# Performance work log

Measured on AMD Instinct MI355X. Metric: run time of the kernel, lower is better.

The kernel has to match this reference:

```python
import jax, jax.numpy as jnp
import numpy as np

N = 50000
F_IN = 512
H1, C1 = 8, 16          # layer-1 heads / per-head channels
H2, C2 = 1, 40          # layer-2 heads / num_classes
NEG_SLOPE = 0.2


def setup_inputs() -> dict:
    key = jax.random.key(0)
    ks = jax.random.split(key, 10)
    E = 800000
    x = jax.random.normal(ks[0], (N, F_IN), dtype=jnp.float32)
    edge_index = jax.random.randint(ks[1], (2, E), 0, N, dtype=jnp.int64)
    s1 = 1.0 / np.sqrt(F_IN)
    s2 = 1.0 / np.sqrt(H1 * C1)
    return {
        "x": x,
        "edge_index": edge_index,
        "W1": jax.random.normal(ks[2], (F_IN, H1 * C1), dtype=jnp.float32) * s1,
        "att_src1": jax.random.normal(ks[3], (H1, C1), dtype=jnp.float32) * s2,
        "att_dst1": jax.random.normal(ks[4], (H1, C1), dtype=jnp.float32) * s2,
        "b1": jnp.zeros((H1 * C1,), dtype=jnp.float32),
        "W2": jax.random.normal(ks[5], (H1 * C1, H2 * C2), dtype=jnp.float32) * s2,
        "att_src2": jax.random.normal(ks[6], (H2, C2), dtype=jnp.float32) * (1.0 / np.sqrt(C2)),
        "att_dst2": jax.random.normal(ks[7], (H2, C2), dtype=jnp.float32) * (1.0 / np.sqrt(C2)),
        "b2": jnp.zeros((H2 * C2,), dtype=jnp.float32),
    }


def _gat_conv(x, W, att_src, att_dst, b, src, dst, H, C):
    # x: [N, Fin] -> h: [N, H, C]
    h = (x @ W).reshape(N, H, C)
    a_src = jnp.einsum("nhc,hc->nh", h, att_src)  # [N, H]
    a_dst = jnp.einsum("nhc,hc->nh", h, att_dst)
    e = a_src[src] + a_dst[dst]                    # [E, H]
    e = jax.nn.leaky_relu(e, NEG_SLOPE)
    # segment softmax over edges sharing the same target node (dst)
    m = jax.ops.segment_max(e, dst, num_segments=N)         # [N, H]
    ex = jnp.exp(e - m[dst])
    denom = jax.ops.segment_sum(ex, dst, num_segments=N)    # [N, H]
    alpha = ex / (denom[dst] + 1e-16)                        # [E, H]
    msg = h[src] * alpha[..., None]                          # [E, H, C]
    out = jax.ops.segment_sum(msg, dst, num_segments=N)     # [N, H, C]
    return out.reshape(N, H * C) + b


def reference(x, edge_index, W1, att_src1, att_dst1, b1, W2, att_src2, att_dst2, b2):
    # add self-loops (PyG GATConv default)
    loop = jnp.arange(N, dtype=edge_index.dtype)
    src = jnp.concatenate([edge_index[0], loop])
    dst = jnp.concatenate([edge_index[1], loop])
    h = _gat_conv(x, W1, att_src1, att_dst1, b1, src, dst, H1, C1)
    h = jax.nn.elu(h)
    h = _gat_conv(h, W2, att_src2, att_dst2, b2, src, dst, H2, C2)
    return jax.nn.log_softmax(h, axis=1)
```

## Files before the change

### kernel.cpp

```cpp
#include <hip/hip_runtime.h>
#include <math.h>

#define N_NODES 50000
#define FIN 512
#define NE 800000
#define ETOT 850000
#define F1 128
#define H1 8
#define F2 40
#define BCAP 64
#define NBIN 196
#define BINCAP 6144

typedef __attribute__((ext_vector_type(8))) short bf16x8;
typedef __attribute__((ext_vector_type(4))) float f32x4;

__device__ inline ushort f2bf(float f){
  union{float f; unsigned u;} v; v.f=f;
  return (ushort)((v.u + 0x8000u) >> 16);
}
__device__ inline float bflo(uint u){ union{uint a;float f;} v; v.a = u << 16;         return v.f; }
__device__ inline float bfhi(uint u){ union{uint a;float f;} v; v.a = u & 0xffff0000u; return v.f; }
__device__ inline float bf1(ushort u){ union{uint a;float f;} v; v.a = ((uint)u) << 16; return v.f; }

__device__ inline bf16x8 cvt8(float4 a, float4 b){
  union{ushort u[8]; bf16x8 v;} r;
  r.u[0]=f2bf(a.x); r.u[1]=f2bf(a.y); r.u[2]=f2bf(a.z); r.u[3]=f2bf(a.w);
  r.u[4]=f2bf(b.x); r.u[5]=f2bf(b.y); r.u[6]=f2bf(b.z); r.u[7]=f2bf(b.w);
  return r.v;
}


__global__ __launch_bounds__(1024) void k_binA(const int* __restrict__ src, const int* __restrict__ dst,
                                               int* __restrict__ binCursor, uint* __restrict__ binbuf){
  __shared__ int hist[256];
  __shared__ int base[256];
  int t = threadIdx.x;
  if(t < 256) hist[t] = 0;
  __syncthreads();

  uint pk[8]; int bn[8];
  int i0 = blockIdx.x*8192 + t;
  #pragma unroll
  for(int k=0;k<8;k++){
    int i = i0 + k*1024;
    int d = -1, s = 0;
    if(i < NE){ d = dst[i]; s = src[i]; }
    else if(i < ETOT){ d = i - NE; s = d; }
    if(d >= 0){
      bn[k] = d >> 8;
      pk[k] = ((uint)d << 16) | (uint)s;
      atomicAdd(&hist[bn[k]], 1);
    } else bn[k] = -1;
  }
  __syncthreads();
  if(t < 256){
    int h = hist[t];
    base[t] = (t < NBIN && h > 0) ? atomicAdd(&binCursor[t], h) : 0;
  }
  __syncthreads();
  if(t < 256) hist[t] = 0;
  __syncthreads();
  #pragma unroll
  for(int k=0;k<8;k++){
    if(bn[k] >= 0){
      int off = atomicAdd(&hist[bn[k]], 1);
      binbuf[(size_t)bn[k]*BINCAP + base[bn[k]] + off] = pk[k];
    }
  }
}


__global__ __launch_bounds__(1024) void k_binB(const int* __restrict__ binCursor, const uint* __restrict__ binbuf,
                                               int* __restrict__ cnt, ushort* __restrict__ bucket){
  __shared__ int lcnt[256];
  __shared__ ushort lb[256][BCAP];
  int b = blockIdx.x, t = threadIdx.x;
  if(t < 256) lcnt[t] = 0;
  __syncthreads();
  int m = min(binCursor[b], BINCAP);
  const uint* p = binbuf + (size_t)b*BINCAP;
  for(int i=t; i<m; i+=1024){
    uint pk = p[i];
    int dl = (pk >> 16) & 255;
    int pos = atomicAdd(&lcnt[dl], 1);
    if(pos < BCAP) lb[dl][pos] = (ushort)(pk & 0xFFFF);
  }
  __syncthreads();
  int n0 = b << 8;
  int nrows = min(256, N_NODES - n0);
  if(t < nrows) cnt[n0 + t] = lcnt[t];
  const uint4* s4 = (const uint4*)lb;
  uint4* d4 = (uint4*)(bucket + (size_t)n0*BCAP);
  int total = nrows * 8;
  for(int i=t; i<total; i+=1024) d4[i] = s4[i];
}


__global__ __launch_bounds__(256) void k_cvtW12(const float* __restrict__ W1, const float* __restrict__ W2,
                                                ushort* __restrict__ Wtb, ushort* __restrict__ Wt2){
  int id = blockIdx.x*256 + threadIdx.x;
  if(id < 65536){
    int k = id >> 7, n = id & 127;
    Wtb[(size_t)(k>>3)*1024 + n*8 + (k&7)] = f2bf(W1[id]);
  } else {
    int id2 = id - 65536;
    if(id2 >= 6144) return;
    int j = id2 & 7;
    int t = id2 >> 3;
    int n = t % 48;
    int t2 = t / 48;
    int quad = t2 & 3, ks = t2 >> 2;
    int k = ks*32 + quad*8 + j;
    Wt2[id2] = (n < F2) ? f2bf(W2[k*F2 + n]) : (ushort)0;
  }
}


__global__ __launch_bounds__(256) void k_gemm1(const float* __restrict__ x, const ushort* __restrict__ Wtb,
                                               const float* __restrict__ as_w, const float* __restrict__ ad_w,
                                               ushort* __restrict__ h1b,
                                               float* __restrict__ a_src, float* __restrict__ a_dst){
  __shared__ ushort Asm[2][32][72];
  int tid  = threadIdx.x;
  int wave = tid >> 6, lane = tid & 63;
  int l15 = lane & 15, quad = lane >> 4;
  int bx = blockIdx.x;

  f32x4 acc[2][2];
  #pragma unroll
  for(int i=0;i<2;i++)
    #pragma unroll
    for(int j=0;j<2;j++) acc[i][j] = (f32x4){0.f,0.f,0.f,0.f};

  int am  = tid >> 3;
  int ak8 = (tid & 7) << 3;
  int agr = bx*32 + am;
  int agrc = min(agr, N_NODES-1);
  const float* xrow = x + (size_t)agrc*FIN + ak8;

  {
    float4 a0 = *(const float4*)xrow;
    float4 a1 = *(const float4*)(xrow + 4);
    *(bf16x8*)&Asm[0][am][ak8] = cvt8(a0, a1);
  }

  const ushort* wpB = Wtb + (size_t)quad*1024 + (size_t)(wave*32 + l15)*8;

  bf16x8 bcur[2][2];
  #pragma unroll
  for(int ks=0;ks<2;ks++)
    #pragma unroll
    for(int tn=0;tn<2;tn++)
      bcur[ks][tn] = *(const bf16x8*)(wpB + ks*4096 + tn*128);
  __syncthreads();

  for(int kt=0; kt<FIN; kt+=64){
    int cur = (kt >> 6) & 1;
    bool hn = (kt + 64) < FIN;

    float4 a0, a1;
    if(hn){
      a0 = *(const float4*)(xrow + kt + 64);
      a1 = *(const float4*)(xrow + kt + 68);
    }
    bf16x8 bnext[2][2];
    if(hn){
      #pragma unroll
      for(int ks=0;ks<2;ks++)
        #pragma unroll
        for(int tn=0;tn<2;tn++)
          bnext[ks][tn] = *(const bf16x8*)(wpB + (size_t)(kt+64)*128 + ks*4096 + tn*128);
    }

    bf16x8 af[2][2];
    #pragma unroll
    for(int tm=0;tm<2;tm++)
      #pragma unroll
      for(int ks=0;ks<2;ks++)
        af[tm][ks] = *(bf16x8*)&Asm[cur][tm*16 + l15][ks*32 + quad*8];

    #pragma unroll
    for(int ks=0;ks<2;ks++)
      #pragma unroll
      for(int tm=0;tm<2;tm++)
        #pragma unroll
        for(int tn=0;tn<2;tn++)
          acc[tm][tn] = __builtin_amdgcn_mfma_f32_16x16x32_bf16(af[tm][ks], bcur[ks][tn], acc[tm][tn], 0,0,0);

    if(hn)
      *(bf16x8*)&Asm[cur^1][am][ak8] = cvt8(a0, a1);
    __syncthreads();
    #pragma unroll
    for(int ks=0;ks<2;ks++)
      #pragma unroll
      for(int tn=0;tn<2;tn++)
        bcur[ks][tn] = bnext[ks][tn];
  }

  float wsv[2], wdv[2];
  #pragma unroll
  for(int tn=0;tn<2;tn++){
    int h = wave*2 + tn;
    wsv[tn] = as_w[h*16 + l15];
    wdv[tn] = ad_w[h*16 + l15];
  }

  #pragma unroll
  for(int tm=0;tm<2;tm++){
    #pragma unroll
    for(int r=0;r<4;r++){
      int row = bx*32 + tm*16 + quad*4 + r;
      bool ok = row < N_NODES;
      #pragma unroll
      for(int tn=0;tn<2;tn++){
        float v = acc[tm][tn][r];
        if(ok){
          int col = wave*32 + tn*16 + l15;
          h1b[(size_t)row*F1 + col] = f2bf(v);
        }
        float ss = v * wsv[tn];
        float dd = v * wdv[tn];
        #pragma unroll
        for(int m=8;m;m>>=1){ ss += __shfl_xor(ss, m); dd += __shfl_xor(dd, m); }
        if(ok && l15 == 0){
          int h = wave*2 + tn;
          a_src[(size_t)row*H1 + h] = ss;
          a_dst[(size_t)row*H1 + h] = dd;
        }
      }
    }
  }
}


__global__ __launch_bounds__(256) void k_agg1(const ushort* __restrict__ h1b, const float* __restrict__ a_src,
                                              const float* __restrict__ a_dst,
                                              const int* __restrict__ cnt, const ushort* __restrict__ bucket,
                                              const float* __restrict__ b1, ushort* __restrict__ gb){
  int wave = threadIdx.x >> 6, lane = threadIdx.x & 63;
  int n = blockIdx.x*4 + wave;
  if(n >= N_NODES) return;
  int hl = lane >> 3;
  float adv = a_dst[n*H1 + hl];
  int deg = min(cnt[n], BCAP);
  int sv = (int)bucket[(n << 6) + lane];
  const uint* h1u = (const uint*)h1b;

  float ws0=0.f, ax0=0.f, ay0=0.f;
  float ws1=0.f, ax1=0.f, ay1=0.f;
  float ws2=0.f, ax2=0.f, ay2=0.f;
  float ws3=0.f, ax3=0.f, ay3=0.f;
  int j = 0;
  for(; j+3<deg; j+=4){
    int s0 = __shfl(sv, j),   s1 = __shfl(sv, j+1);
    int s2 = __shfl(sv, j+2), s3 = __shfl(sv, j+3);
    float e0 = a_src[s0*H1 + hl] + adv;
    float e1 = a_src[s1*H1 + hl] + adv;
    float e2 = a_src[s2*H1 + hl] + adv;
    float e3 = a_src[s3*H1 + hl] + adv;
    e0 = e0 > 0.f ? e0 : 0.2f*e0;  e1 = e1 > 0.f ? e1 : 0.2f*e1;
    e2 = e2 > 0.f ? e2 : 0.2f*e2;  e3 = e3 > 0.f ? e3 : 0.2f*e3;
    float w0=__expf(e0), w1=__expf(e1), w2=__expf(e2), w3=__expf(e3);
    uint u0 = h1u[(size_t)s0*64 + lane];
    uint u1 = h1u[(size_t)s1*64 + lane];
    uint u2 = h1u[(size_t)s2*64 + lane];
    uint u3 = h1u[(size_t)s3*64 + lane];
    ax0 += w0*bflo(u0); ay0 += w0*bfhi(u0); ws0 += w0;
    ax1 += w1*bflo(u1); ay1 += w1*bfhi(u1); ws1 += w1;
    ax2 += w2*bflo(u2); ay2 += w2*bfhi(u2); ws2 += w2;
    ax3 += w3*bflo(u3); ay3 += w3*bfhi(u3); ws3 += w3;
  }
  for(; j<deg; j++){
    int s0 = __shfl(sv, j);
    float e0 = a_src[s0*H1 + hl] + adv;
    e0 = e0 > 0.f ? e0 : 0.2f*e0;
    float w0 = __expf(e0);
    uint u0 = h1u[(size_t)s0*64 + lane];
    ax0 += w0*bflo(u0); ay0 += w0*bfhi(u0); ws0 += w0;
  }
  float wsum = (ws0+ws1)+(ws2+ws3);
  float inv = 1.f/(wsum + 1e-16f);
  int c0 = lane*2;
  float o0 = ((ax0+ax1)+(ax2+ax3))*inv + b1[c0];
  float o1 = ((ay0+ay1)+(ay2+ay3))*inv + b1[c0+1];
  o0 = o0 > 0.f ? o0 : expm1f(o0);
  o1 = o1 > 0.f ? o1 : expm1f(o1);
  uint up = (uint)f2bf(o0) | ((uint)f2bf(o1) << 16);
  ((uint*)gb)[(size_t)n*64 + lane] = up;
}


__global__ __launch_bounds__(256) void k_gemm2(const ushort* __restrict__ gb, const ushort* __restrict__ Wt2,
                                               const float* __restrict__ as_w, const float* __restrict__ ad_w,
                                               ushort* __restrict__ h2b,
                                               float* __restrict__ a_src, float* __restrict__ a_dst){
  int tid = threadIdx.x;
  int wave = tid >> 6, lane = tid & 63;
  int l15 = lane & 15, quad = lane >> 4;
  int row0 = blockIdx.x*64 + wave*16;
  int arow = min(row0 + l15, N_NODES-1);
  const ushort* ap = gb + (size_t)arow*F1 + quad*8;

  f32x4 acc[3];
  #pragma unroll
  for(int tn=0;tn<3;tn++) acc[tn] = (f32x4){0.f,0.f,0.f,0.f};

  #pragma unroll
  for(int ks=0;ks<4;ks++){
    bf16x8 af = *(const bf16x8*)(ap + ks*32);
    #pragma unroll
    for(int tn=0;tn<3;tn++){
      bf16x8 bf = *(const bf16x8*)(Wt2 + ((size_t)(ks*4+quad)*48 + tn*16 + l15)*8);
      acc[tn] = __builtin_amdgcn_mfma_f32_16x16x32_bf16(af, bf, acc[tn], 0,0,0);
    }
  }

  float ws2v[3], wd2v[3];
  #pragma unroll
  for(int tn=0;tn<3;tn++){
    int col = tn*16 + l15;
    ws2v[tn] = (col < F2) ? as_w[col] : 0.f;
    wd2v[tn] = (col < F2) ? ad_w[col] : 0.f;
  }

  #pragma unroll
  for(int r=0;r<4;r++){
    int row = row0 + quad*4 + r;
    bool ok = row < N_NODES;
    float ss = 0.f, dd = 0.f;
    #pragma unroll
    for(int tn=0;tn<3;tn++){
      float v = acc[tn][r];
      int col = tn*16 + l15;
      if(ok && col < F2) h2b[(size_t)row*F2 + col] = f2bf(v);
      ss += v * ws2v[tn];
      dd += v * wd2v[tn];
    }
    #pragma unroll
    for(int m=8;m;m>>=1){ ss += __shfl_xor(ss, m); dd += __shfl_xor(dd, m); }
    if(ok && l15 == 0){
      a_src[row] = ss;
      a_dst[row] = dd;
    }
  }
}


__global__ __launch_bounds__(256) void k_agg2(const ushort* __restrict__ h2b, const float* __restrict__ a_src,
                                              const float* __restrict__ a_dst,
                                              const int* __restrict__ cnt, const ushort* __restrict__ bucket,
                                              const float* __restrict__ b2, float* __restrict__ out){
  int wave = threadIdx.x >> 6, lane = threadIdx.x & 63;
  int n = blockIdx.x*4 + wave;
  if(n >= N_NODES) return;
  float adv = a_dst[n];
  int deg = min(cnt[n], BCAP);
  int sv = (int)bucket[(n << 6) + lane];
  int c = (lane < F2) ? lane : (F2-1);

  float ws0=0.f, ac0=0.f, ws1=0.f, ac1=0.f, ws2=0.f, ac2=0.f, ws3=0.f, ac3=0.f;
  int j = 0;
  for(; j+3<deg; j+=4){
    int s0 = __shfl(sv, j),   s1 = __shfl(sv, j+1);
    int s2 = __shfl(sv, j+2), s3 = __shfl(sv, j+3);
    float e0 = a_src[s0] + adv, e1 = a_src[s1] + adv;
    float e2 = a_src[s2] + adv, e3 = a_src[s3] + adv;
    e0 = e0 > 0.f ? e0 : 0.2f*e0;  e1 = e1 > 0.f ? e1 : 0.2f*e1;
    e2 = e2 > 0.f ? e2 : 0.2f*e2;  e3 = e3 > 0.f ? e3 : 0.2f*e3;
    float w0=__expf(e0), w1=__expf(e1), w2=__expf(e2), w3=__expf(e3);
    ac0 += w0*bf1(h2b[(size_t)s0*F2 + c]); ws0 += w0;
    ac1 += w1*bf1(h2b[(size_t)s1*F2 + c]); ws1 += w1;
    ac2 += w2*bf1(h2b[(size_t)s2*F2 + c]); ws2 += w2;
    ac3 += w3*bf1(h2b[(size_t)s3*F2 + c]); ws3 += w3;
  }
  for(; j<deg; j++){
    int s0 = __shfl(sv, j);
    float e0 = a_src[s0] + adv;
    e0 = e0 > 0.f ? e0 : 0.2f*e0;
    float w0 = __expf(e0);
    ac0 += w0*bf1(h2b[(size_t)s0*F2 + c]); ws0 += w0;
  }
  float v = ((ac0+ac1)+(ac2+ac3))/(((ws0+ws1)+(ws2+ws3)) + 1e-16f) + b2[c];
  float mv = (lane < F2) ? v : -INFINITY;
  #pragma unroll
  for(int off=32; off; off>>=1) mv = fmaxf(mv, __shfl_xor(mv, off));
  float ex = (lane < F2) ? __expf(v - mv) : 0.f;
  #pragma unroll
  for(int off=32; off; off>>=1) ex += __shfl_xor(ex, off);
  if(lane < F2) out[(size_t)n*F2 + lane] = v - mv - logf(ex);
}


extern "C" void kernel_launch(void* const* d_in, const int* in_sizes, int n_in,
                              void* d_out, int out_size, void* d_ws, size_t ws_size,
                              hipStream_t stream) {
  const float* x        = (const float*)d_in[0];
  const int*   eidx     = (const int*)d_in[1];
  const float* W1       = (const float*)d_in[2];
  const float* att_src1 = (const float*)d_in[3];
  const float* att_dst1 = (const float*)d_in[4];
  const float* b1       = (const float*)d_in[5];
  const float* W2       = (const float*)d_in[6];
  const float* att_src2 = (const float*)d_in[7];
  const float* att_dst2 = (const float*)d_in[8];
  const float* b2       = (const float*)d_in[9];
  float* out = (float*)d_out;

  const int* src = eidx;
  const int* dst = eidx + NE;

  ushort* h1b  = (ushort*)d_ws;
  ushort* h2b  = h1b + 6400000;
  ushort* gb   = h2b + 2000000;
  ushort* Wtb  = gb + 6400000;
  ushort* bucket = Wtb + 65536;
  float* a_src1 = (float*)(bucket + 3200000);
  float* a_dst1 = a_src1 + 400000;
  float* a_src2 = a_dst1 + 400000;
  float* a_dst2 = a_src2 + 50000;
  int* cnt      = (int*)(a_dst2 + 50000);
  int* binCursor= cnt + 50002;
  uint* binbuf  = (uint*)(binCursor + 256);
  ushort* Wt2   = (ushort*)(binbuf + (size_t)NBIN*BINCAP);

  hipMemsetAsync(binCursor, 0, NBIN*sizeof(int), stream);
  k_binA<<<(ETOT+8191)/8192, 1024, 0, stream>>>(src, dst, binCursor, binbuf);
  k_binB<<<NBIN, 1024, 0, stream>>>(binCursor, binbuf, cnt, bucket);

  k_cvtW12<<<280, 256, 0, stream>>>(W1, W2, Wtb, Wt2);
  k_gemm1 <<<(N_NODES+31)/32, 256, 0, stream>>>(x, Wtb, att_src1, att_dst1, h1b, a_src1, a_dst1);
  k_agg1  <<<(N_NODES+3)/4, 256, 0, stream>>>(h1b, a_src1, a_dst1, cnt, bucket, b1, gb);

  k_gemm2 <<<(N_NODES+63)/64, 256, 0, stream>>>(gb, Wt2, att_src2, att_dst2, h2b, a_src2, a_dst2);
  k_agg2  <<<(N_NODES+3)/4, 256, 0, stream>>>(h2b, a_src2, a_dst2, cnt, bucket, b2, out);
}
```

Baseline: 289.3 us.

## Split each node's edge aggregation across four waves with LDS reduction

Both aggregation kernels now assign one block per destination node instead of one wave per node. The node's edge list is split evenly across the four waves, and their partial sums are combined through shared memory before wave 0 finishes the normalisation and writes the output. The aim is more memory-level parallelism per node and shorter serial gather chains. The cost is a block-wide barrier per node, a quarter as many nodes per block, and fewer edges per wave (about 17 per node on average) to amortise the per-node setup.

```diff
diff --git a/kernel.cpp b/kernel.cpp
--- a/kernel.cpp
+++ b/kernel.cpp
@@ -238,8 +238,9 @@
                                               const float* __restrict__ a_dst,
                                               const int* __restrict__ cnt, const ushort* __restrict__ bucket,
                                               const float* __restrict__ b1, ushort* __restrict__ gb){
+  __shared__ float pws[4][64], pax[4][64], pay[4][64];
   int wave = threadIdx.x >> 6, lane = threadIdx.x & 63;
-  int n = blockIdx.x*4 + wave;
+  int n = blockIdx.x;
   if(n >= N_NODES) return;
   int hl = lane >> 3;
   float adv = a_dst[n*H1 + hl];
@@ -247,12 +248,15 @@
   int sv = (int)bucket[(n << 6) + lane];
   const uint* h1u = (const uint*)h1b;
 
+  int q  = (deg + 3) >> 2;
+  int j0 = wave*q, j1 = min(j0 + q, deg);
+
   float ws0=0.f, ax0=0.f, ay0=0.f;
   float ws1=0.f, ax1=0.f, ay1=0.f;
   float ws2=0.f, ax2=0.f, ay2=0.f;
   float ws3=0.f, ax3=0.f, ay3=0.f;
-  int j = 0;
-  for(; j+3<deg; j+=4){
+  int j = j0;
+  for(; j+3<j1; j+=4){
     int s0 = __shfl(sv, j),   s1 = __shfl(sv, j+1);
     int s2 = __shfl(sv, j+2), s3 = __shfl(sv, j+3);
     float e0 = a_src[s0*H1 + hl] + adv;
@@ -271,7 +275,7 @@
     ax2 += w2*bflo(u2); ay2 += w2*bfhi(u2); ws2 += w2;
     ax3 += w3*bflo(u3); ay3 += w3*bfhi(u3); ws3 += w3;
   }
-  for(; j<deg; j++){
+  for(; j<j1; j++){
     int s0 = __shfl(sv, j);
     float e0 = a_src[s0*H1 + hl] + adv;
     e0 = e0 > 0.f ? e0 : 0.2f*e0;
@@ -279,15 +283,23 @@
     uint u0 = h1u[(size_t)s0*64 + lane];
     ax0 += w0*bflo(u0); ay0 += w0*bfhi(u0); ws0 += w0;
   }
-  float wsum = (ws0+ws1)+(ws2+ws3);
-  float inv = 1.f/(wsum + 1e-16f);
-  int c0 = lane*2;
-  float o0 = ((ax0+ax1)+(ax2+ax3))*inv + b1[c0];
-  float o1 = ((ay0+ay1)+(ay2+ay3))*inv + b1[c0+1];
-  o0 = o0 > 0.f ? o0 : expm1f(o0);
-  o1 = o1 > 0.f ? o1 : expm1f(o1);
-  uint up = (uint)f2bf(o0) | ((uint)f2bf(o1) << 16);
-  ((uint*)gb)[(size_t)n*64 + lane] = up;
+  pws[wave][lane] = (ws0+ws1)+(ws2+ws3);
+  pax[wave][lane] = (ax0+ax1)+(ax2+ax3);
+  pay[wave][lane] = (ay0+ay1)+(ay2+ay3);
+  __syncthreads();
+  if(wave == 0){
+    float W  = (pws[0][lane]+pws[1][lane]) + (pws[2][lane]+pws[3][lane]);
+    float AX = (pax[0][lane]+pax[1][lane]) + (pax[2][lane]+pax[3][lane]);
+    float AY = (pay[0][lane]+pay[1][lane]) + (pay[2][lane]+pay[3][lane]);
+    float inv = 1.f/(W + 1e-16f);
+    int c0 = lane*2;
+    float o0 = AX*inv + b1[c0];
+    float o1 = AY*inv + b1[c0+1];
+    o0 = o0 > 0.f ? o0 : expm1f(o0);
+    o1 = o1 > 0.f ? o1 : expm1f(o1);
+    uint up = (uint)f2bf(o0) | ((uint)f2bf(o1) << 16);
+    ((uint*)gb)[(size_t)n*64 + lane] = up;
+  }
 }
 
 
@@ -351,17 +363,21 @@
                                               const float* __restrict__ a_dst,
                                               const int* __restrict__ cnt, const ushort* __restrict__ bucket,
                                               const float* __restrict__ b2, float* __restrict__ out){
+  __shared__ float pws[4][64], pac[4][64];
   int wave = threadIdx.x >> 6, lane = threadIdx.x & 63;
-  int n = blockIdx.x*4 + wave;
+  int n = blockIdx.x;
   if(n >= N_NODES) return;
   float adv = a_dst[n];
   int deg = min(cnt[n], BCAP);
   int sv = (int)bucket[(n << 6) + lane];
   int c = (lane < F2) ? lane : (F2-1);
 
+  int q  = (deg + 3) >> 2;
+  int j0 = wave*q, j1 = min(j0 + q, deg);
+
   float ws0=0.f, ac0=0.f, ws1=0.f, ac1=0.f, ws2=0.f, ac2=0.f, ws3=0.f, ac3=0.f;
-  int j = 0;
-  for(; j+3<deg; j+=4){
+  int j = j0;
+  for(; j+3<j1; j+=4){
     int s0 = __shfl(sv, j),   s1 = __shfl(sv, j+1);
     int s2 = __shfl(sv, j+2), s3 = __shfl(sv, j+3);
     float e0 = a_src[s0] + adv, e1 = a_src[s1] + adv;
@@ -374,21 +390,28 @@
     ac2 += w2*bf1(h2b[(size_t)s2*F2 + c]); ws2 += w2;
     ac3 += w3*bf1(h2b[(size_t)s3*F2 + c]); ws3 += w3;
   }
-  for(; j<deg; j++){
+  for(; j<j1; j++){
     int s0 = __shfl(sv, j);
     float e0 = a_src[s0] + adv;
     e0 = e0 > 0.f ? e0 : 0.2f*e0;
     float w0 = __expf(e0);
     ac0 += w0*bf1(h2b[(size_t)s0*F2 + c]); ws0 += w0;
   }
-  float v = ((ac0+ac1)+(ac2+ac3))/(((ws0+ws1)+(ws2+ws3)) + 1e-16f) + b2[c];
-  float mv = (lane < F2) ? v : -INFINITY;
-  #pragma unroll
-  for(int off=32; off; off>>=1) mv = fmaxf(mv, __shfl_xor(mv, off));
-  float ex = (lane < F2) ? __expf(v - mv) : 0.f;
-  #pragma unroll
-  for(int off=32; off; off>>=1) ex += __shfl_xor(ex, off);
-  if(lane < F2) out[(size_t)n*F2 + lane] = v - mv - logf(ex);
+  pws[wave][lane] = (ws0+ws1)+(ws2+ws3);
+  pac[wave][lane] = (ac0+ac1)+(ac2+ac3);
+  __syncthreads();
+  if(wave == 0){
+    float W = (pws[0][lane]+pws[1][lane]) + (pws[2][lane]+pws[3][lane]);
+    float A = (pac[0][lane]+pac[1][lane]) + (pac[2][lane]+pac[3][lane]);
+    float v = A/(W + 1e-16f) + b2[c];
+    float mv = (lane < F2) ? v : -INFINITY;
+    #pragma unroll
+    for(int off=32; off; off>>=1) mv = fmaxf(mv, __shfl_xor(mv, off));
+    float ex = (lane < F2) ? __expf(v - mv) : 0.f;
+    #pragma unroll
+    for(int off=32; off; off>>=1) ex += __shfl_xor(ex, off);
+    if(lane < F2) out[(size_t)n*F2 + lane] = v - mv - logf(ex);
+  }
 }
 
 
@@ -430,8 +453,8 @@
 
   k_cvtW12<<<280, 256, 0, stream>>>(W1, W2, Wtb, Wt2);
   k_gemm1 <<<(N_NODES+31)/32, 256, 0, stream>>>(x, Wtb, att_src1, att_dst1, h1b, a_src1, a_dst1);
-  k_agg1  <<<(N_NODES+3)/4, 256, 0, stream>>>(h1b, a_src1, a_dst1, cnt, bucket, b1, gb);
+  k_agg1  <<<N_NODES, 256, 0, stream>>>(h1b, a_src1, a_dst1, cnt, bucket, b1, gb);
 
   k_gemm2 <<<(N_NODES+63)/64, 256, 0, stream>>>(gb, Wt2, att_src2, att_dst2, h2b, a_src2, a_dst2);
-  k_agg2  <<<(N_NODES+3)/4, 256, 0, stream>>>(h2b, a_src2, a_dst2, cnt, bucket, b2, out);
-}
+  k_agg2  <<<N_NODES, 256, 0, stream>>>(h2b, a_src2, a_dst2, cnt, bucket, b2, out);
+}
```

New measurement: 320.2 us. 10.7% more time.

## Replace two-pass binned edge bucketing with single-pass global atomic bucketing

Applied to the files above, without the earlier changes.

Drops the two-kernel scheme (binA scatters packed edges into 256-node bins, binB sorts each bin in shared memory and writes buckets). A single kernel now does one global atomicAdd per edge on the per-node count and writes the source index straight into that node's bucket slot. This removes a launch, the intermediate bin buffer round trip and the shared-memory staging, but adds about 850k contended global atomics and scattered 2-byte writes. Slot order within a bucket becomes nondeterministic.

```diff
diff --git a/kernel.cpp b/kernel.cpp
--- a/kernel.cpp
+++ b/kernel.cpp
@@ -9,8 +9,6 @@
 #define H1 8
 #define F2 40
 #define BCAP 64
-#define NBIN 196
-#define BINCAP 6144
 
 typedef __attribute__((ext_vector_type(8))) short bf16x8;
 typedef __attribute__((ext_vector_type(4))) float f32x4;
@@ -31,69 +29,15 @@
 }
 
 
-__global__ __launch_bounds__(1024) void k_binA(const int* __restrict__ src, const int* __restrict__ dst,
-                                               int* __restrict__ binCursor, uint* __restrict__ binbuf){
-  __shared__ int hist[256];
-  __shared__ int base[256];
-  int t = threadIdx.x;
-  if(t < 256) hist[t] = 0;
-  __syncthreads();
-
-  uint pk[8]; int bn[8];
-  int i0 = blockIdx.x*8192 + t;
-  #pragma unroll
-  for(int k=0;k<8;k++){
-    int i = i0 + k*1024;
-    int d = -1, s = 0;
-    if(i < NE){ d = dst[i]; s = src[i]; }
-    else if(i < ETOT){ d = i - NE; s = d; }
-    if(d >= 0){
-      bn[k] = d >> 8;
-      pk[k] = ((uint)d << 16) | (uint)s;
-      atomicAdd(&hist[bn[k]], 1);
-    } else bn[k] = -1;
-  }
-  __syncthreads();
-  if(t < 256){
-    int h = hist[t];
-    base[t] = (t < NBIN && h > 0) ? atomicAdd(&binCursor[t], h) : 0;
-  }
-  __syncthreads();
-  if(t < 256) hist[t] = 0;
-  __syncthreads();
-  #pragma unroll
-  for(int k=0;k<8;k++){
-    if(bn[k] >= 0){
-      int off = atomicAdd(&hist[bn[k]], 1);
-      binbuf[(size_t)bn[k]*BINCAP + base[bn[k]] + off] = pk[k];
-    }
-  }
-}
-
-
-__global__ __launch_bounds__(1024) void k_binB(const int* __restrict__ binCursor, const uint* __restrict__ binbuf,
-                                               int* __restrict__ cnt, ushort* __restrict__ bucket){
-  __shared__ int lcnt[256];
-  __shared__ ushort lb[256][BCAP];
-  int b = blockIdx.x, t = threadIdx.x;
-  if(t < 256) lcnt[t] = 0;
-  __syncthreads();
-  int m = min(binCursor[b], BINCAP);
-  const uint* p = binbuf + (size_t)b*BINCAP;
-  for(int i=t; i<m; i+=1024){
-    uint pk = p[i];
-    int dl = (pk >> 16) & 255;
-    int pos = atomicAdd(&lcnt[dl], 1);
-    if(pos < BCAP) lb[dl][pos] = (ushort)(pk & 0xFFFF);
-  }
-  __syncthreads();
-  int n0 = b << 8;
-  int nrows = min(256, N_NODES - n0);
-  if(t < nrows) cnt[n0 + t] = lcnt[t];
-  const uint4* s4 = (const uint4*)lb;
-  uint4* d4 = (uint4*)(bucket + (size_t)n0*BCAP);
-  int total = nrows * 8;
-  for(int i=t; i<total; i+=1024) d4[i] = s4[i];
+__global__ __launch_bounds__(256) void k_bucket(const int* __restrict__ src, const int* __restrict__ dst,
+                                                int* __restrict__ cnt, ushort* __restrict__ bucket){
+  int i = blockIdx.x*256 + threadIdx.x;
+  if(i >= ETOT) return;
+  int d, s;
+  if(i < NE){ d = dst[i]; s = src[i]; }
+  else      { d = i - NE; s = d; }
+  int pos = atomicAdd(&cnt[d], 1);
+  if(pos < BCAP) bucket[(d << 6) + pos] = (ushort)s;
 }
 
 
@@ -420,13 +364,10 @@
   float* a_src2 = a_dst1 + 400000;
   float* a_dst2 = a_src2 + 50000;
   int* cnt      = (int*)(a_dst2 + 50000);
-  int* binCursor= cnt + 50002;
-  uint* binbuf  = (uint*)(binCursor + 256);
-  ushort* Wt2   = (ushort*)(binbuf + (size_t)NBIN*BINCAP);
-
-  hipMemsetAsync(binCursor, 0, NBIN*sizeof(int), stream);
-  k_binA<<<(ETOT+8191)/8192, 1024, 0, stream>>>(src, dst, binCursor, binbuf);
-  k_binB<<<NBIN, 1024, 0, stream>>>(binCursor, binbuf, cnt, bucket);
+  ushort* Wt2   = (ushort*)(cnt + 50002);
+
+  hipMemsetAsync(cnt, 0, N_NODES*sizeof(int), stream);
+  k_bucket<<<(ETOT+255)/256, 256, 0, stream>>>(src, dst, cnt, bucket);
 
   k_cvtW12<<<280, 256, 0, stream>>>(W1, W2, Wtb, Wt2);
   k_gemm1 <<<(N_NODES+31)/32, 256, 0, stream>>>(x, Wtb, att_src1, att_dst1, h1b, a_src1, a_dst1);
```

New measurement: 312.8 us. 8.1% more time.

## Fuse binning with weight conversion and bucket build with GEMM1 into shared launches

Applied to the files above, without the earlier changes.

Merges the edge-binning pass and the weight bf16 conversion into one kernel with block-range dispatch. It also merges the per-bin bucket build with the first GEMM, packing four 256-thread GEMM tiles into each 1024-thread block. The aim is to cut kernel launches and let independent stages overlap on the GPU. In exchange, the shared-memory footprint per block grows and block-wide barriers now span four independent tiles, which may reduce GEMM occupancy.

```diff
diff --git a/kernel.cpp b/kernel.cpp
--- a/kernel.cpp
+++ b/kernel.cpp
@@ -31,101 +31,109 @@
 }
 
 
-__global__ __launch_bounds__(1024) void k_binA(const int* __restrict__ src, const int* __restrict__ dst,
-                                               int* __restrict__ binCursor, uint* __restrict__ binbuf){
+__global__ __launch_bounds__(1024) void k_pro(const int* __restrict__ src, const int* __restrict__ dst,
+                                              int* __restrict__ binCursor, uint* __restrict__ binbuf,
+                                              const float* __restrict__ W1, const float* __restrict__ W2,
+                                              ushort* __restrict__ Wtb, ushort* __restrict__ Wt2){
   __shared__ int hist[256];
   __shared__ int base[256];
-  int t = threadIdx.x;
-  if(t < 256) hist[t] = 0;
-  __syncthreads();
-
-  uint pk[8]; int bn[8];
-  int i0 = blockIdx.x*8192 + t;
-  #pragma unroll
-  for(int k=0;k<8;k++){
-    int i = i0 + k*1024;
-    int d = -1, s = 0;
-    if(i < NE){ d = dst[i]; s = src[i]; }
-    else if(i < ETOT){ d = i - NE; s = d; }
-    if(d >= 0){
-      bn[k] = d >> 8;
-      pk[k] = ((uint)d << 16) | (uint)s;
-      atomicAdd(&hist[bn[k]], 1);
-    } else bn[k] = -1;
-  }
-  __syncthreads();
-  if(t < 256){
-    int h = hist[t];
-    base[t] = (t < NBIN && h > 0) ? atomicAdd(&binCursor[t], h) : 0;
-  }
-  __syncthreads();
-  if(t < 256) hist[t] = 0;
-  __syncthreads();
-  #pragma unroll
-  for(int k=0;k<8;k++){
-    if(bn[k] >= 0){
-      int off = atomicAdd(&hist[bn[k]], 1);
-      binbuf[(size_t)bn[k]*BINCAP + base[bn[k]] + off] = pk[k];
-    }
-  }
-}
-
-
-__global__ __launch_bounds__(1024) void k_binB(const int* __restrict__ binCursor, const uint* __restrict__ binbuf,
-                                               int* __restrict__ cnt, ushort* __restrict__ bucket){
+  int bx = blockIdx.x, t = threadIdx.x;
+
+  if(bx < 104){
+    if(t < 256) hist[t] = 0;
+    __syncthreads();
+
+    uint pk[8]; int bn[8];
+    int i0 = bx*8192 + t;
+    #pragma unroll
+    for(int k=0;k<8;k++){
+      int i = i0 + k*1024;
+      int d = -1, s = 0;
+      if(i < NE){ d = dst[i]; s = src[i]; }
+      else if(i < ETOT){ d = i - NE; s = d; }
+      if(d >= 0){
+        bn[k] = d >> 8;
+        pk[k] = ((uint)d << 16) | (uint)s;
+        atomicAdd(&hist[bn[k]], 1);
+      } else bn[k] = -1;
+    }
+    __syncthreads();
+    if(t < 256){
+      int h = hist[t];
+      base[t] = (t < NBIN && h > 0) ? atomicAdd(&binCursor[t], h) : 0;
+    }
+    __syncthreads();
+    if(t < 256) hist[t] = 0;
+    __syncthreads();
+    #pragma unroll
+    for(int k=0;k<8;k++){
+      if(bn[k] >= 0){
+        int off = atomicAdd(&hist[bn[k]], 1);
+        binbuf[(size_t)bn[k]*BINCAP + base[bn[k]] + off] = pk[k];
+      }
+    }
+  } else {
+    int id = (bx - 104)*1024 + t;
+    if(id < 65536){
+      int k = id >> 7, n = id & 127;
+      Wtb[(size_t)(k>>3)*1024 + n*8 + (k&7)] = f2bf(W1[id]);
+    } else {
+      int id2 = id - 65536;
+      if(id2 < 6144){
+        int j = id2 & 7;
+        int tt = id2 >> 3;
+        int n = tt % 48;
+        int t2 = tt / 48;
+        int quad = t2 & 3, ks = t2 >> 2;
+        int k = ks*32 + quad*8 + j;
+        Wt2[id2] = (n < F2) ? f2bf(W2[k*F2 + n]) : (ushort)0;
+      }
+    }
+  }
+}
+
+
+__global__ __launch_bounds__(1024) void k_g1b(const int* __restrict__ binCursor, const uint* __restrict__ binbuf,
+                                              int* __restrict__ cnt, ushort* __restrict__ bucket,
+                                              const float* __restrict__ x, const ushort* __restrict__ Wtb,
+                                              const float* __restrict__ as_w, const float* __restrict__ ad_w,
+                                              ushort* __restrict__ h1b,
+                                              float* __restrict__ a_src, float* __restrict__ a_dst){
   __shared__ int lcnt[256];
   __shared__ ushort lb[256][BCAP];
-  int b = blockIdx.x, t = threadIdx.x;
-  if(t < 256) lcnt[t] = 0;
-  __syncthreads();
-  int m = min(binCursor[b], BINCAP);
-  const uint* p = binbuf + (size_t)b*BINCAP;
-  for(int i=t; i<m; i+=1024){
-    uint pk = p[i];
-    int dl = (pk >> 16) & 255;
-    int pos = atomicAdd(&lcnt[dl], 1);
-    if(pos < BCAP) lb[dl][pos] = (ushort)(pk & 0xFFFF);
-  }
-  __syncthreads();
-  int n0 = b << 8;
-  int nrows = min(256, N_NODES - n0);
-  if(t < nrows) cnt[n0 + t] = lcnt[t];
-  const uint4* s4 = (const uint4*)lb;
-  uint4* d4 = (uint4*)(bucket + (size_t)n0*BCAP);
-  int total = nrows * 8;
-  for(int i=t; i<total; i+=1024) d4[i] = s4[i];
-}
-
-
-__global__ __launch_bounds__(256) void k_cvtW12(const float* __restrict__ W1, const float* __restrict__ W2,
-                                                ushort* __restrict__ Wtb, ushort* __restrict__ Wt2){
-  int id = blockIdx.x*256 + threadIdx.x;
-  if(id < 65536){
-    int k = id >> 7, n = id & 127;
-    Wtb[(size_t)(k>>3)*1024 + n*8 + (k&7)] = f2bf(W1[id]);
-  } else {
-    int id2 = id - 65536;
-    if(id2 >= 6144) return;
-    int j = id2 & 7;
-    int t = id2 >> 3;
-    int n = t % 48;
-    int t2 = t / 48;
-    int quad = t2 & 3, ks = t2 >> 2;
-    int k = ks*32 + quad*8 + j;
-    Wt2[id2] = (n < F2) ? f2bf(W2[k*F2 + n]) : (ushort)0;
-  }
-}
-
-
-__global__ __launch_bounds__(256) void k_gemm1(const float* __restrict__ x, const ushort* __restrict__ Wtb,
-                                               const float* __restrict__ as_w, const float* __restrict__ ad_w,
-                                               ushort* __restrict__ h1b,
-                                               float* __restrict__ a_src, float* __restrict__ a_dst){
-  __shared__ ushort Asm[2][32][72];
-  int tid  = threadIdx.x;
+  __shared__ ushort Asm[4][2][32][72];
+  int bxg = blockIdx.x;
+
+  if(bxg < NBIN){
+    int b = bxg, t = threadIdx.x;
+    if(t < 256) lcnt[t] = 0;
+    __syncthreads();
+    int m = min(binCursor[b], BINCAP);
+    const uint* p = binbuf + (size_t)b*BINCAP;
+    for(int i=t; i<m; i+=1024){
+      uint pk = p[i];
+      int dl = (pk >> 16) & 255;
+      int pos = atomicAdd(&lcnt[dl], 1);
+      if(pos < BCAP) lb[dl][pos] = (ushort)(pk & 0xFFFF);
+    }
+    __syncthreads();
+    int n0 = b << 8;
+    int nrows = min(256, N_NODES - n0);
+    if(t < nrows) cnt[n0 + t] = lcnt[t];
+    const uint4* s4 = (const uint4*)lb;
+    uint4* d4 = (uint4*)(bucket + (size_t)n0*BCAP);
+    int total = nrows * 8;
+    for(int i=t; i<total; i+=1024) d4[i] = s4[i];
+    return;
+  }
+
+  int sub = threadIdx.x >> 8;
+  int tid = threadIdx.x & 255;
+  int tileIdx = (bxg - NBIN)*4 + sub;
+  int bx = min(tileIdx, 1562);
+
   int wave = tid >> 6, lane = tid & 63;
   int l15 = lane & 15, quad = lane >> 4;
-  int bx = blockIdx.x;
 
   f32x4 acc[2][2];
   #pragma unroll
@@ -142,7 +150,7 @@
   {
     float4 a0 = *(const float4*)xrow;
     float4 a1 = *(const float4*)(xrow + 4);
-    *(bf16x8*)&Asm[0][am][ak8] = cvt8(a0, a1);
+    *(bf16x8*)&Asm[sub][0][am][ak8] = cvt8(a0, a1);
   }
 
   const ushort* wpB = Wtb + (size_t)quad*1024 + (size_t)(wave*32 + l15)*8;
@@ -178,7 +186,7 @@
     for(int tm=0;tm<2;tm++)
       #pragma unroll
       for(int ks=0;ks<2;ks++)
-        af[tm][ks] = *(bf16x8*)&Asm[cur][tm*16 + l15][ks*32 + quad*8];
+        af[tm][ks] = *(bf16x8*)&Asm[sub][cur][tm*16 + l15][ks*32 + quad*8];
 
     #pragma unroll
     for(int ks=0;ks<2;ks++)
@@ -189,7 +197,7 @@
           acc[tm][tn] = __builtin_amdgcn_mfma_f32_16x16x32_bf16(af[tm][ks], bcur[ks][tn], acc[tm][tn], 0,0,0);
 
     if(hn)
-      *(bf16x8*)&Asm[cur^1][am][ak8] = cvt8(a0, a1);
+      *(bf16x8*)&Asm[sub][cur^1][am][ak8] = cvt8(a0, a1);
     __syncthreads();
     #pragma unroll
     for(int ks=0;ks<2;ks++)
@@ -425,13 +433,14 @@
   ushort* Wt2   = (ushort*)(binbuf + (size_t)NBIN*BINCAP);
 
   hipMemsetAsync(binCursor, 0, NBIN*sizeof(int), stream);
-  k_binA<<<(ETOT+8191)/8192, 1024, 0, stream>>>(src, dst, binCursor, binbuf);
-  k_binB<<<NBIN, 1024, 0, stream>>>(binCursor, binbuf, cnt, bucket);
-
-  k_cvtW12<<<280, 256, 0, stream>>>(W1, W2, Wtb, Wt2);
-  k_gemm1 <<<(N_NODES+31)/32, 256, 0, stream>>>(x, Wtb, att_src1, att_dst1, h1b, a_src1, a_dst1);
-  k_agg1  <<<(N_NODES+3)/4, 256, 0, stream>>>(h1b, a_src1, a_dst1, cnt, bucket, b1, gb);
-
-  k_gemm2 <<<(N_NODES+63)/64, 256, 0, stream>>>(gb, Wt2, att_src2, att_dst2, h2b, a_src2, a_dst2);
-  k_agg2  <<<(N_NODES+3)/4, 256, 0, stream>>>(h2b, a_src2, a_dst2, cnt, bucket, b2, out);
-}
+
+  k_pro<<<174, 1024, 0, stream>>>(src, dst, binCursor, binbuf, W1, W2, Wtb, Wt2);
+
+  k_g1b<<<NBIN + 391, 1024, 0, stream>>>(binCursor, binbuf, cnt, bucket,
+                                         x, Wtb, att_src1, att_dst1, h1b, a_src1, a_dst1);
+
+  k_agg1<<<(N_NODES+3)/4, 256, 0, stream>>>(h1b, a_src1, a_dst1, cnt, bucket, b1, gb);
+
+  k_gemm2<<<(N_NODES+63)/64, 256, 0, stream>>>(gb, Wt2, att_src2, att_dst2, h2b, a_src2, a_dst2);
+  k_agg2 <<<(N_NODES+3)/4, 256, 0, stream>>>(h2b, a_src2, a_dst2, cnt, bucket, b2, out);
+}
```

After: 285.5 us. About the same (-1.3%).
